# Kernel optimization log

Hardware: AMD Instinct MI355X
Metric: run time of the kernel (lower is better)

## Reference

```python
import jax, jax.numpy as jnp
import numpy as np

B, S, D, H = 4, 2048, 1024, 16
HD = D // H  # head_dim = 64


def setup_inputs() -> dict:
    key = jax.random.key(0)
    ks = jax.random.split(key, 5)
    scale = 0.02
    return {
        "x": jax.random.normal(ks[0], (B, S, D), dtype=jnp.float32),
        "Wq": jax.random.normal(ks[1], (D, D), dtype=jnp.float32) * scale,
        "Wk": jax.random.normal(ks[2], (D, D), dtype=jnp.float32) * scale,
        "Wv": jax.random.normal(ks[3], (D, D), dtype=jnp.float32) * scale,
        "Wo": jax.random.normal(ks[4], (D, D), dtype=jnp.float32) * scale,
        "bo": jnp.zeros((D,), dtype=jnp.float32),
    }


def reference(x, Wq, Wk, Wv, Wo, bo):
    b, s, d = x.shape
    # projections (no bias on q/k/v, matching qkv_bias=False)
    q = (x @ Wq).reshape(b, s, H, HD).transpose(0, 2, 1, 3)  # [B,H,S,HD]
    k = (x @ Wk).reshape(b, s, H, HD).transpose(0, 2, 1, 3)
    v = (x @ Wv).reshape(b, s, H, HD).transpose(0, 2, 1, 3)
    scores = jnp.einsum("bhqd,bhkd->bhqk", q, k) / jnp.sqrt(jnp.float32(HD))
    causal = jnp.tril(jnp.ones((s, s), dtype=bool))  # True = keep
    scores = jnp.where(causal, scores, -jnp.inf)
    attn = jax.nn.softmax(scores, axis=-1)
    # dropout p=0.0 -> identity
    out = jnp.einsum("bhqk,bhkd->bhqd", attn, v)
    out = out.transpose(0, 2, 1, 3).reshape(b, s, d)
    return out @ Wo + bo
```

## Files before the change

### kernel.cpp

```cpp
#include <hip/hip_runtime.h>

typedef unsigned short u16;
typedef unsigned int u32;
typedef __attribute__((ext_vector_type(4))) float f32x4;
typedef __attribute__((ext_vector_type(8))) __bf16 bf16x8;
typedef __attribute__((ext_vector_type(4))) _Float16 f16x4;
typedef __attribute__((ext_vector_type(4))) u16 u16x4;
typedef __attribute__((ext_vector_type(4))) u32 u32x4;
typedef __attribute__((ext_vector_type(2))) u32 u32x2;

#define D_ 1024
#define S_ 2048
#define B_ 4
#define H_ 16
#define HD_ 64
#define M_ 8192
#define LDP 72
#define QSCALE 0.18033688011112042591f

__device__ __forceinline__ u16 f2bf(float f) {
  u32 u = __float_as_uint(f);
  u += 0x7fffu + ((u >> 16) & 1u);
  return (u16)(u >> 16);
}

__device__ __forceinline__ float max3f(float a, float b, float c) {
  return fmaxf(fmaxf(a, b), c);
}

__global__ __launch_bounds__(256) void cast_x_kernel(const float* __restrict__ x,
                                                     u16* __restrict__ xb) {
  int i = (blockIdx.x * 256 + threadIdx.x) * 4;
  f32x4 v = *(const f32x4*)(x + i);
  u16x4 o = {f2bf(v[0]), f2bf(v[1]), f2bf(v[2]), f2bf(v[3])};
  *(u16x4*)(xb + i) = o;
}

__global__ __launch_bounds__(256) void wtrans_kernel(const float* __restrict__ Wq, const float* __restrict__ Wk,
                                                     const float* __restrict__ Wv, const float* __restrict__ Wo,
                                                     u16* __restrict__ Wqt, u16* __restrict__ Wkt,
                                                     u16* __restrict__ Wvt, u16* __restrict__ Wot) {
  __shared__ float lds[64][65];
  const float* W = blockIdx.z == 0 ? Wq : blockIdx.z == 1 ? Wk : blockIdx.z == 2 ? Wv : Wo;
  u16* Wt       = blockIdx.z == 0 ? Wqt : blockIdx.z == 1 ? Wkt : blockIdx.z == 2 ? Wvt : Wot;
  int k0 = blockIdx.x * 64, n0 = blockIdx.y * 64;
  int tr = threadIdx.x >> 6, tc = threadIdx.x & 63;
#pragma unroll
  for (int i = 0; i < 16; ++i)
    lds[tr + i * 4][tc] = W[(size_t)(k0 + tr + i * 4) * D_ + n0 + tc];
  __syncthreads();
#pragma unroll
  for (int i = 0; i < 16; ++i)
    Wt[(size_t)(n0 + tr + i * 4) * D_ + k0 + tc] = f2bf(lds[tc][tr + i * 4]);
}

__device__ __forceinline__ void gemm_main(const u16* __restrict__ A, const u16* __restrict__ Bt,
                                          u16* As, u16* Bs, int row0, int col0, f32x4 acc[4][4]) {
  const int tid = threadIdx.x;
  const int lane = tid & 63, wave = tid >> 6;
  const int wr = wave >> 1, wc = wave & 1;
  const int l15 = lane & 15, lg = lane >> 4;
#pragma unroll 1
  for (int k0 = 0; k0 < D_; k0 += 64) {
    __syncthreads();
#pragma unroll
    for (int it = 0; it < 4; ++it) {
      int idx = it * 256 + tid;
      int r = idx >> 3, c = (idx & 7) << 3;
      *(u32x4*)(As + r * LDP + c) = *(const u32x4*)(A + (size_t)(row0 + r) * D_ + k0 + c);
      *(u32x4*)(Bs + r * LDP + c) = *(const u32x4*)(Bt + (size_t)(col0 + r) * D_ + k0 + c);
    }
    __syncthreads();
#pragma unroll
    for (int kk = 0; kk < 64; kk += 32) {
      bf16x8 af[4], bf[4];
#pragma unroll
      for (int m = 0; m < 4; ++m)
        af[m] = *(const bf16x8*)(As + (wr * 64 + m * 16 + l15) * LDP + kk + lg * 8);
#pragma unroll
      for (int n = 0; n < 4; ++n)
        bf[n] = *(const bf16x8*)(Bs + (wc * 64 + n * 16 + l15) * LDP + kk + lg * 8);
#pragma unroll
      for (int m = 0; m < 4; ++m)
#pragma unroll
        for (int n = 0; n < 4; ++n)
          acc[m][n] = __builtin_amdgcn_mfma_f32_16x16x32_bf16(af[m], bf[n], acc[m][n], 0, 0, 0);
    }
  }
}

__global__ __launch_bounds__(256) void qkv_gemm_kernel(const u16* __restrict__ xb,
                                                       const u16* __restrict__ Wqt, const u16* __restrict__ Wkt,
                                                       const u16* __restrict__ Wvt,
                                                       u16* __restrict__ Qb, u16* __restrict__ Kb,
                                                       _Float16* __restrict__ Vt) {
  __shared__ u16 As[128 * LDP];
  __shared__ u16 Bs[128 * LDP];
  int lin = blockIdx.x;
  int xcd = lin & 7, pos = lin >> 3;
  int mode = pos / 64;
  int rem = pos & 63;
  int by = xcd * 8 + (rem >> 3);
  int bx = rem & 7;
  const u16* Bt = mode == 0 ? Wqt : mode == 1 ? Wkt : Wvt;
  f32x4 acc[4][4] = {};
  int row0 = by * 128, col0 = bx * 128;
  gemm_main(xb, Bt, As, Bs, row0, col0, acc);
  int lane = threadIdx.x & 63, wave = threadIdx.x >> 6;
  int wr = wave >> 1, wc = wave & 1, l15 = lane & 15, lg = lane >> 4;
  int rbase = row0 + wr * 64 + lg * 4, cbase = col0 + wc * 64 + l15;
  if (mode == 2) {
#pragma unroll
    for (int m = 0; m < 4; ++m) {
      int row = rbase + m * 16;
      int b = row >> 11, s = row & (S_ - 1);
#pragma unroll
      for (int n = 0; n < 4; ++n) {
        int col = cbase + n * 16;
        int h = col >> 6, hd = col & 63;
        f16x4 vv = {(_Float16)acc[m][n][0], (_Float16)acc[m][n][1],
                    (_Float16)acc[m][n][2], (_Float16)acc[m][n][3]};
        *(f16x4*)(Vt + ((size_t)((b << 4) + h) * HD_ + hd) * S_ + s) = vv;
      }
    }
  } else {
    u16* dst = mode == 0 ? Qb : Kb;
    float scl = mode == 0 ? QSCALE : 1.0f;
#pragma unroll
    for (int m = 0; m < 4; ++m)
#pragma unroll
      for (int n = 0; n < 4; ++n) {
        int col = cbase + n * 16;
#pragma unroll
        for (int r = 0; r < 4; ++r) {
          int row = rbase + m * 16 + r;
          dst[(size_t)row * D_ + col] = f2bf(acc[m][n][r] * scl);
        }
      }
  }
}

__global__ __launch_bounds__(256) void attn_kernel(const u16* __restrict__ Qb, const u16* __restrict__ Kb,
                                                   const _Float16* __restrict__ Vt, u16* __restrict__ attnb) {
  __shared__ u16 Ks[2][64][LDP];
  __shared__ _Float16 Vs[2][HD_][LDP];
  const int tid = threadIdx.x;
  const int wave = tid >> 6, lane = tid & 63;
  const int l15 = lane & 15, lg = lane >> 4;
  const int lin = blockIdx.x;
  const int xcd = lin & 7, slot = lin >> 3;
  const int p = slot >> 3;
  const int bh = (slot & 7) * 8 + xcd;
  const int b = bh >> 4, h = bh & 15;

  const int srow = tid >> 3;
  const int scol = (tid & 7) * 8;
  const u16* Kg = Kb + (size_t)(b * S_) * D_ + h * HD_;
  const _Float16* Vg = Vt + (size_t)bh * HD_ * S_;

  const f16x4 ones16 = {(_Float16)1.0f, (_Float16)1.0f, (_Float16)1.0f, (_Float16)1.0f};

#pragma unroll 1
  for (int phase = 0; phase < 2; ++phase) {
    const int qblk = phase == 0 ? (31 - p) : p;
    const int q0b = qblk * 64;
    const int ntiles = qblk + 1;
    const int q0 = q0b + wave * 16;

    const u16* Qrow = Qb + (size_t)(b * S_ + q0 + l15) * D_ + h * HD_;
    bf16x8 qf0 = *(const bf16x8*)(Qrow + lg * 8);
    bf16x8 qf1 = *(const bf16x8*)(Qrow + 32 + lg * 8);

    float m = -1e30f;
    f32x4 o[4] = {};
    f32x4 osum = {};
    u32x4 kreg0, kreg1, vreg0, vreg1;

    __syncthreads();
    kreg0 = *(const u32x4*)(Kg + (size_t)(srow) * D_ + scol);
    kreg1 = *(const u32x4*)(Kg + (size_t)(32 + srow) * D_ + scol);
    vreg0 = *(const u32x4*)(Vg + (size_t)srow * S_ + scol);
    vreg1 = *(const u32x4*)(Vg + (size_t)(32 + srow) * S_ + scol);
    *(u32x4*)(&Ks[0][srow][scol]) = kreg0;
    *(u32x4*)(&Ks[0][32 + srow][scol]) = kreg1;
    *(u32x4*)(&Vs[0][srow][scol]) = vreg0;
    *(u32x4*)(&Vs[0][32 + srow][scol]) = vreg1;

#pragma unroll 1
    for (int t = 0; t < ntiles; ++t) {
      const int cur = t & 1;
      __syncthreads();
      if (t + 1 < ntiles) {
        int kv0n = (t + 1) * 64;
        kreg0 = *(const u32x4*)(Kg + (size_t)(kv0n + srow) * D_ + scol);
        kreg1 = *(const u32x4*)(Kg + (size_t)(kv0n + 32 + srow) * D_ + scol);
        vreg0 = *(const u32x4*)(Vg + (size_t)srow * S_ + kv0n + scol);
        vreg1 = *(const u32x4*)(Vg + (size_t)(32 + srow) * S_ + kv0n + scol);
      }
      f32x4 s[4];
      __builtin_amdgcn_s_setprio(1);
#pragma unroll
      for (int j = 0; j < 4; ++j) {
        bf16x8 kf0 = *(const bf16x8*)(&Ks[cur][j * 16 + l15][lg * 8]);
        bf16x8 kf1 = *(const bf16x8*)(&Ks[cur][j * 16 + l15][32 + lg * 8]);
        f32x4 z = {0.f, 0.f, 0.f, 0.f};
        z = __builtin_amdgcn_mfma_f32_16x16x32_bf16(kf0, qf0, z, 0, 0, 0);
        z = __builtin_amdgcn_mfma_f32_16x16x32_bf16(kf1, qf1, z, 0, 0, 0);
        s[j] = z;
      }
      __builtin_amdgcn_s_setprio(0);
      if (t == ntiles - 1) {
        int qr = wave * 16 + l15;
#pragma unroll
        for (int j = 0; j < 4; ++j)
#pragma unroll
          for (int r = 0; r < 4; ++r)
            if (j * 16 + lg * 4 + r > qr) s[j][r] = -1e30f;
      }
      float x0 = max3f(s[0][0], s[0][1], s[0][2]);
      float x1 = max3f(s[0][3], s[1][0], s[1][1]);
      float x2 = max3f(s[1][2], s[1][3], s[2][0]);
      float x3 = max3f(s[2][1], s[2][2], s[2][3]);
      float x4 = max3f(s[3][0], s[3][1], s[3][2]);
      float tmax = fmaxf(max3f(x0, x1, x2), max3f(x3, x4, s[3][3]));
      tmax = fmaxf(tmax, __shfl_xor(tmax, 16));
      tmax = fmaxf(tmax, __shfl_xor(tmax, 32));
      if (!__all(tmax - m <= 8.f)) {
        float nm = fmaxf(m, tmax);
        float alpha = exp2f(m - nm);
        m = nm;
        osum *= alpha;
#pragma unroll
        for (int hf = 0; hf < 4; ++hf) o[hf] *= alpha;
      }
      f16x4 pb[4];
#pragma unroll
      for (int j = 0; j < 4; ++j) {
        float p0 = exp2f(s[j][0] - m), p1 = exp2f(s[j][1] - m);
        float p2 = exp2f(s[j][2] - m), p3 = exp2f(s[j][3] - m);
        u32 lo = __builtin_bit_cast(u32, __builtin_amdgcn_cvt_pkrtz(p0, p1));
        u32 hi = __builtin_bit_cast(u32, __builtin_amdgcn_cvt_pkrtz(p2, p3));
        pb[j] = __builtin_bit_cast(f16x4, (u32x2){lo, hi});
      }
      __builtin_amdgcn_s_setprio(1);
#pragma unroll
      for (int j = 0; j < 4; ++j) {
#pragma unroll
        for (int hf = 0; hf < 4; ++hf) {
          f16x4 vf = *(const f16x4*)(&Vs[cur][hf * 16 + l15][j * 16 + lg * 4]);
          o[hf] = __builtin_amdgcn_mfma_f32_16x16x16f16(vf, pb[j], o[hf], 0, 0, 0);
        }
        osum = __builtin_amdgcn_mfma_f32_16x16x16f16(ones16, pb[j], osum, 0, 0, 0);
      }
      __builtin_amdgcn_s_setprio(0);
      if (t + 1 < ntiles) {
        const int nxt = cur ^ 1;
        *(u32x4*)(&Ks[nxt][srow][scol]) = kreg0;
        *(u32x4*)(&Ks[nxt][32 + srow][scol]) = kreg1;
        *(u32x4*)(&Vs[nxt][srow][scol]) = vreg0;
        *(u32x4*)(&Vs[nxt][32 + srow][scol]) = vreg1;
      }
    }
    float inv = 1.0f / osum[0];
    u16* Orow = attnb + (size_t)(b * S_ + q0 + l15) * D_ + h * HD_ + lg * 4;
#pragma unroll
    for (int hf = 0; hf < 4; ++hf) {
      u16x4 ov = {f2bf(o[hf][0] * inv), f2bf(o[hf][1] * inv),
                  f2bf(o[hf][2] * inv), f2bf(o[hf][3] * inv)};
      *(u16x4*)(Orow + hf * 16) = ov;
    }
  }
}

__global__ __launch_bounds__(256) void out_gemm_kernel(const u16* __restrict__ attnb, const u16* __restrict__ Wot,
                                                       const float* __restrict__ bo, float* __restrict__ outp) {
  __shared__ u16 As[128 * LDP];
  __shared__ u16 Bs[128 * LDP];
  int lin = blockIdx.x;
  int xcd = lin & 7, pos = lin >> 3;
  int by = xcd * 8 + (pos >> 3);
  int bx = pos & 7;
  f32x4 acc[4][4] = {};
  int row0 = by * 128, col0 = bx * 128;
  gemm_main(attnb, Wot, As, Bs, row0, col0, acc);
  int lane = threadIdx.x & 63, wave = threadIdx.x >> 6;
  int wr = wave >> 1, wc = wave & 1, l15 = lane & 15, lg = lane >> 4;
  int rbase = row0 + wr * 64 + lg * 4, cbase = col0 + wc * 64 + l15;
#pragma unroll
  for (int n = 0; n < 4; ++n) {
    float bn = bo[cbase + n * 16];
#pragma unroll
    for (int m = 0; m < 4; ++m)
#pragma unroll
      for (int r = 0; r < 4; ++r)
        outp[(size_t)(rbase + m * 16 + r) * D_ + cbase + n * 16] = acc[m][n][r] + bn;
  }
}

extern "C" void kernel_launch(void* const* d_in, const int* in_sizes, int n_in,
                              void* d_out, int out_size, void* d_ws, size_t ws_size,
                              hipStream_t stream) {
  const float* x  = (const float*)d_in[0];
  const float* Wq = (const float*)d_in[1];
  const float* Wk = (const float*)d_in[2];
  const float* Wv = (const float*)d_in[3];
  const float* Wo = (const float*)d_in[4];
  const float* bo = (const float*)d_in[5];
  float* outp = (float*)d_out;

  char* ws = (char*)d_ws;
  u16* xb        = (u16*)(ws);
  u16* Wqt       = (u16*)(ws + ((size_t)16 << 20));
  u16* Wkt       = (u16*)(ws + ((size_t)18 << 20));
  u16* Wvt       = (u16*)(ws + ((size_t)20 << 20));
  u16* Wot       = (u16*)(ws + ((size_t)22 << 20));
  u16* Qb        = (u16*)(ws + ((size_t)24 << 20));
  u16* Kb        = (u16*)(ws + ((size_t)40 << 20));
  _Float16* Vt   = (_Float16*)(ws + ((size_t)56 << 20));
  u16* attnb     = (u16*)(ws + ((size_t)72 << 20));

  cast_x_kernel<<<dim3(M_ * D_ / (256 * 4)), dim3(256), 0, stream>>>(x, xb);
  wtrans_kernel<<<dim3(16, 16, 4), dim3(256), 0, stream>>>(Wq, Wk, Wv, Wo, Wqt, Wkt, Wvt, Wot);
  qkv_gemm_kernel<<<dim3(1536), dim3(256), 0, stream>>>(xb, Wqt, Wkt, Wvt, Qb, Kb, Vt);
  attn_kernel<<<dim3(1024), dim3(256), 0, stream>>>(Qb, Kb, Vt, attnb);
  out_gemm_kernel<<<dim3(512), dim3(256), 0, stream>>>(attnb, Wot, bo, outp);
}
```

Measured before the change: 215.7 us.

## Load GEMM tiles via direct global-to-LDS loads with XOR-swizzled layout

Replaces the register-staged global->LDS copy in the shared GEMM main loop with global_load_lds 16-byte direct transfers. Padded rows become an unpadded 64-wide layout with an XOR swizzle on the 8-element chunk index to avoid bank conflicts. This removes VGPR round-trips and LDS write instructions and shrinks LDS use, which could raise occupancy. Correctness depends on the per-wave direct-LDS addressing matching the swizzled read pattern, and there is still no double buffering.

```diff
diff --git a/kernel.cpp b/kernel.cpp
--- a/kernel.cpp
+++ b/kernel.cpp
@@ -26,6 +26,11 @@
 
 __device__ __forceinline__ float max3f(float a, float b, float c) {
   return fmaxf(fmaxf(a, b), c);
+}
+
+__device__ __forceinline__ void gload_lds16(const void* g, void* l) {
+  __builtin_amdgcn_global_load_lds((const __attribute__((address_space(1))) void*)g,
+                                   (__attribute__((address_space(3))) void*)l, 16, 0, 0);
 }
 
 __global__ __launch_bounds__(256) void cast_x_kernel(const float* __restrict__ x,
@@ -60,32 +65,39 @@
   const int lane = tid & 63, wave = tid >> 6;
   const int wr = wave >> 1, wc = wave & 1;
   const int l15 = lane & 15, lg = lane >> 4;
+  const int sr8 = lane >> 3;
+  const int scx = (lane & 7) ^ sr8;
 #pragma unroll 1
   for (int k0 = 0; k0 < D_; k0 += 64) {
+#pragma unroll
+    for (int it = 0; it < 4; ++it) {
+      int rbase = (it * 4 + wave) * 8;
+      int r = rbase + sr8;
+      gload_lds16(A + (size_t)(row0 + r) * D_ + k0 + scx * 8, As + rbase * 64);
+      gload_lds16(Bt + (size_t)(col0 + r) * D_ + k0 + scx * 8, Bs + rbase * 64);
+    }
     __syncthreads();
 #pragma unroll
-    for (int it = 0; it < 4; ++it) {
-      int idx = it * 256 + tid;
-      int r = idx >> 3, c = (idx & 7) << 3;
-      *(u32x4*)(As + r * LDP + c) = *(const u32x4*)(A + (size_t)(row0 + r) * D_ + k0 + c);
-      *(u32x4*)(Bs + r * LDP + c) = *(const u32x4*)(Bt + (size_t)(col0 + r) * D_ + k0 + c);
-    }
-    __syncthreads();
-#pragma unroll
     for (int kk = 0; kk < 64; kk += 32) {
+      const int cb = kk >> 3;
       bf16x8 af[4], bf[4];
 #pragma unroll
-      for (int m = 0; m < 4; ++m)
-        af[m] = *(const bf16x8*)(As + (wr * 64 + m * 16 + l15) * LDP + kk + lg * 8);
-#pragma unroll
-      for (int n = 0; n < 4; ++n)
-        bf[n] = *(const bf16x8*)(Bs + (wc * 64 + n * 16 + l15) * LDP + kk + lg * 8);
+      for (int m = 0; m < 4; ++m) {
+        int row = wr * 64 + m * 16 + l15;
+        af[m] = *(const bf16x8*)(As + row * 64 + (((cb + lg) ^ (l15 & 7)) << 3));
+      }
+#pragma unroll
+      for (int n = 0; n < 4; ++n) {
+        int row = wc * 64 + n * 16 + l15;
+        bf[n] = *(const bf16x8*)(Bs + row * 64 + (((cb + lg) ^ (l15 & 7)) << 3));
+      }
 #pragma unroll
       for (int m = 0; m < 4; ++m)
 #pragma unroll
         for (int n = 0; n < 4; ++n)
           acc[m][n] = __builtin_amdgcn_mfma_f32_16x16x32_bf16(af[m], bf[n], acc[m][n], 0, 0, 0);
     }
+    __syncthreads();
   }
 }
 
@@ -94,8 +106,8 @@
                                                        const u16* __restrict__ Wvt,
                                                        u16* __restrict__ Qb, u16* __restrict__ Kb,
                                                        _Float16* __restrict__ Vt) {
-  __shared__ u16 As[128 * LDP];
-  __shared__ u16 Bs[128 * LDP];
+  __shared__ u16 As[128 * 64];
+  __shared__ u16 Bs[128 * 64];
   int lin = blockIdx.x;
   int xcd = lin & 7, pos = lin >> 3;
   int mode = pos / 64;
@@ -274,8 +286,8 @@
 
 __global__ __launch_bounds__(256) void out_gemm_kernel(const u16* __restrict__ attnb, const u16* __restrict__ Wot,
                                                        const float* __restrict__ bo, float* __restrict__ outp) {
-  __shared__ u16 As[128 * LDP];
-  __shared__ u16 Bs[128 * LDP];
+  __shared__ u16 As[128 * 64];
+  __shared__ u16 Bs[128 * 64];
   int lin = blockIdx.x;
   int xcd = lin & 7, pos = lin >> 3;
   int by = xcd * 8 + (pos >> 3);
```

After: 210.9 us. 1.02x faster.
